# Performance work log

Hardware: AMD Instinct MI355X
Metric: run time of the kernel (lower is better)

## Reference

```python
import jax, jax.numpy as jnp
import numpy as np

D_MODEL = 1024
NUM_HEADS = 16
HEAD_DIM = D_MODEL // NUM_HEADS


def setup_inputs() -> dict:
    key = jax.random.key(0)
    ks = jax.random.split(key, 11)
    B, S = 2, 2048
    sc = 1.0 / np.sqrt(D_MODEL)
    inp = {
        "query": jax.random.normal(ks[0], (B, S, D_MODEL), jnp.float32),
        "key": jax.random.normal(ks[1], (B, S, D_MODEL), jnp.float32),
        "value": jax.random.normal(ks[2], (B, S, D_MODEL), jnp.float32),
        "Wq": jax.random.normal(ks[3], (D_MODEL, D_MODEL), jnp.float32) * sc,
        "bq": jnp.zeros((D_MODEL,), jnp.float32),
        "Wk": jax.random.normal(ks[4], (D_MODEL, D_MODEL), jnp.float32) * sc,
        "bk": jnp.zeros((D_MODEL,), jnp.float32),
        "Wv": jax.random.normal(ks[5], (D_MODEL, D_MODEL), jnp.float32) * sc,
        "bv": jnp.zeros((D_MODEL,), jnp.float32),
        "Wo": jax.random.normal(ks[6], (D_MODEL, D_MODEL), jnp.float32) * sc,
        "bo": jnp.zeros((D_MODEL,), jnp.float32),
    }
    return inp


def _split_heads(x):
    B, S, _ = x.shape
    return x.reshape(B, S, NUM_HEADS, HEAD_DIM).transpose(0, 2, 1, 3)  # [B,H,S,Dh]


def reference(query, key, value, Wq, bq, Wk, bk, Wv, bv, Wo, bo):
    Q = _split_heads(query @ Wq.T + bq)
    K = _split_heads(key @ Wk.T + bk)
    V = _split_heads(value @ Wv.T + bv)
    scores = jnp.einsum("bhqd,bhkd->bhqk", Q, K) / jnp.sqrt(jnp.float32(HEAD_DIM))
    attn = jax.nn.softmax(scores, axis=-1)  # dropout = identity (eval)
    out = jnp.einsum("bhqk,bhkd->bhqd", attn, V)
    B, H, S, Dh = out.shape
    out = out.transpose(0, 2, 1, 3).reshape(B, S, H * Dh)
    return out @ Wo.T + bo
```

## Files before the change

kernel.cpp:

```cpp
#include <hip/hip_runtime.h>
#include <hip/hip_bf16.h>

typedef __attribute__((ext_vector_type(8))) short short8;
typedef __attribute__((ext_vector_type(4))) short short4v;
typedef __attribute__((ext_vector_type(4))) float f32x4;
typedef __attribute__((ext_vector_type(16))) float f32x16;
typedef __attribute__((ext_vector_type(4))) int int4v;
typedef __attribute__((ext_vector_type(2))) int int2v;

#define DEV static __device__ __forceinline__

constexpr int S_LEN   = 2048;
constexpr int DMODEL  = 1024;
constexpr int NHEAD   = 16;
constexpr int DHEAD   = 64;
constexpr int NBATCH  = 2;
constexpr int BHN     = NBATCH * NHEAD;
constexpr int MROWS   = NBATCH * S_LEN;
constexpr int NDIM    = DMODEL;

DEV unsigned short f2b(float f) {
  __hip_bfloat16 h = __float2bfloat16(f);
  return __builtin_bit_cast(unsigned short, h);
}
DEV unsigned pk2(float a, float b) {
  return (unsigned)f2b(a) | ((unsigned)f2b(b) << 16);
}
DEV short8 ld8(const void* p) {
  return *reinterpret_cast<const short8*>(p);
}
DEV f32x4 mfma16(short8 a, short8 b, f32x4 c) {
  return __builtin_amdgcn_mfma_f32_16x16x32_bf16(a, b, c, 0, 0, 0);
}
DEV f32x16 mfma32(short8 a, short8 b, f32x16 c) {
  return __builtin_amdgcn_mfma_f32_32x32x16_bf16(a, b, c, 0, 0, 0);
}
DEV void gload16(const void* g, void* l) {
  __builtin_amdgcn_global_load_lds(
      (const __attribute__((address_space(1))) unsigned*)g,
      (__attribute__((address_space(3))) unsigned*)l, 16, 0, 0);
}

struct CvtArgs {
  const float* src[7];
  unsigned short* dst[7];
  int n4[7];
};

__global__ __launch_bounds__(256) void cvt_bf16(CvtArgs c) {
  const int seg = blockIdx.y;
  const float* __restrict__ s = c.src[seg];
  unsigned short* __restrict__ d = c.dst[seg];
  const int n4 = c.n4[seg];
  for (int i = blockIdx.x * 256 + threadIdx.x; i < n4; i += gridDim.x * 256) {
    f32x4 v = reinterpret_cast<const f32x4*>(s)[i];
    short4v r;
    r[0] = (short)f2b(v[0]); r[1] = (short)f2b(v[1]);
    r[2] = (short)f2b(v[2]); r[3] = (short)f2b(v[3]);
    reinterpret_cast<short4v*>(d)[i] = r;
  }
}

struct GB {
  const unsigned short* A[3];
  const unsigned short* W[3];
  const float* bia[3];
  void* out[3];
  int epi[3];
};

#define WAITV3 asm volatile("s_waitcnt vmcnt(3)" ::: "memory")
#define WAITV0 asm volatile("s_waitcnt vmcnt(0)" ::: "memory")

__global__ __launch_bounds__(256, 4) void gemm_bf16(GB g) {
  const int z = blockIdx.z;
  const unsigned short* __restrict__ A = g.A[z];
  const unsigned short* __restrict__ W = g.W[z];
  const float* __restrict__ bia = g.bia[z];
  const int epi = g.epi[z];
  const int bm = blockIdx.y, bn = blockIdx.x;
  const int tid = threadIdx.x, lane = tid & 63, wid = tid >> 6;
  const int wr = wid >> 1, wc = wid & 1;
  const int fr = lane & 15, gq = lane >> 4;

  __shared__ unsigned short As[3][128][32];
  __shared__ unsigned short Bs[3][64][32];

  f32x4 acc[4][2] = {};

  const int srow = lane >> 2;
  const int scol = ((lane & 3) ^ ((srow >> 1) & 3)) * 16;
  const char* aS = (const char*)A + (size_t)(bm * 128 + wid * 32 + srow) * 2048 + scol;
  const char* bS = (const char*)W + (size_t)(bn * 64 + wid * 16 + srow) * 2048 + scol;

  auto stage = [&](int buf, int kt) {
    const int ko = kt * 64;
    char* a0 = (char*)As[buf] + wid * 2048;
    char* b0 = (char*)Bs[buf] + wid * 1024;
    gload16(aS + ko, a0);
    gload16(aS + (size_t)16 * 2048 + ko, a0 + 1024);
    gload16(bS + ko, b0);
  };

  const int rdo = (gq ^ ((fr >> 1) & 3)) * 8;

  stage(0, 0);
  stage(1, 1);
  for (int kt = 0; kt < 32; ++kt) {
    if (kt < 31) { WAITV3; } else { WAITV0; }
    __builtin_amdgcn_s_barrier();
    if (kt + 2 < 32) stage((kt + 2) % 3, kt + 2);
    const int buf = kt % 3;
    short8 af[4], bf4[2];
#pragma unroll
    for (int i = 0; i < 4; ++i) af[i] = ld8(&As[buf][wr * 64 + i * 16 + fr][rdo]);
#pragma unroll
    for (int j = 0; j < 2; ++j) bf4[j] = ld8(&Bs[buf][wc * 32 + j * 16 + fr][rdo]);
#pragma unroll
    for (int i = 0; i < 4; ++i)
#pragma unroll
      for (int j = 0; j < 2; ++j)
        acc[i][j] = mfma16(af[i], bf4[j], acc[i][j]);
  }

#pragma unroll
  for (int i = 0; i < 4; ++i) {
#pragma unroll
    for (int j = 0; j < 2; ++j) {
#pragma unroll
      for (int r = 0; r < 4; ++r) {
        const int row = bm * 128 + wr * 64 + i * 16 + gq * 4 + r;
        const int col = bn * 64 + wc * 32 + j * 16 + fr;
        float v = acc[i][j][r] + bia[col];
        if (epi == 3) {
          ((float*)g.out[z])[(size_t)row * NDIM + col] = v;
        } else {
          const int b = row >> 11, s = row & (S_LEN - 1);
          const int h = col >> 6,  dh = col & (DHEAD - 1);
          unsigned short* O = (unsigned short*)g.out[z];
          if (epi == 0)      O[((size_t)(b * NHEAD + h) * S_LEN + s) * DHEAD + dh] = f2b(v * 0.125f);
          else if (epi == 1) O[((size_t)(b * NHEAD + h) * S_LEN + s) * DHEAD + dh] = f2b(v);
          else               O[((size_t)(b * NHEAD + h) * DHEAD + dh) * S_LEN + s] = f2b(v);
        }
      }
    }
  }
}

__global__ __launch_bounds__(512, 2) void attn_fwd(
    const unsigned short* __restrict__ Qp,
    const unsigned short* __restrict__ Kp,
    const unsigned short* __restrict__ Vt,
    unsigned short* __restrict__ AO) {
  const int nb = (blockIdx.x & 7) * 64 + (blockIdx.x >> 3);
  const int qt = nb & 15, bh = nb >> 4;
  const int tid = threadIdx.x, lane = tid & 63, wid = tid >> 6;
  const int qw = wid & 3, hw = wid >> 2;
  const int ql = lane & 31, hi = lane >> 5, l7 = lane & 7, l3 = lane >> 3;

  const unsigned short* Qh = Qp + (size_t)bh * S_LEN * DHEAD;
  const char* Kh = (const char*)(Kp + (size_t)bh * S_LEN * DHEAD);
  const char* Vh = (const char*)(Vt + (size_t)bh * DHEAD * S_LEN);

  __shared__ unsigned short Klds[2][2][4096];
  __shared__ unsigned short Vlds[2][2][4096];

  const int q0 = qt * 128 + qw * 32;
  short8 qf[4];
#pragma unroll
  for (int d16 = 0; d16 < 4; ++d16)
    qf[d16] = ld8(Qh + (size_t)(q0 + ql) * DHEAD + d16 * 16 + hi * 8);

  const int swc = (l7 ^ l3) << 4;
  const char* kS = Kh + (size_t)hw * 16 * 8192 + (qw * 16 + l3) * 128 + swc;
  const char* vS = Vh + (size_t)hw * 16 * 128 + (qw * 16 + l3) * 4096 + swc;
  char* kD0 = (char*)Klds[hw][0] + qw * 2048;
  char* vD0 = (char*)Vlds[hw][0] + qw * 2048;
  char* kD1 = (char*)Klds[hw][1] + qw * 2048;
  char* vD1 = (char*)Vlds[hw][1] + qw * 2048;

  int xo[4];
#pragma unroll
  for (int j = 0; j < 4; ++j) xo[j] = ((j * 2 + hi) ^ l7) << 4;

  float m = -1e30f, l = 0.f;
  f32x16 o0 = {}, o1 = {};

  gload16(kS, kD0); gload16(kS + 1024, kD0 + 1024);
  gload16(vS, vD0); gload16(vS + 32768, vD0 + 1024);
  __syncthreads();

  constexpr int NT = S_LEN / 64 / 2;
  for (int kt = 0; kt < NT; ++kt) {
    const int buf = kt & 1;
    if (kt + 1 < NT) {
      const char* kn = kS + (kt + 1) * 8192;
      const char* vn = vS + (kt + 1) * 128;
      char* kD = buf ? kD0 : kD1;
      char* vD = buf ? vD0 : vD1;
      gload16(kn, kD); gload16(kn + 1024, kD + 1024);
      gload16(vn, vD); gload16(vn + 32768, vD + 1024);
    }
    const char* kb = (const char*)Klds[hw][buf] + ql * 128;
    const char* vb = (const char*)Vlds[hw][buf] + ql * 128;

    f32x16 st0 = {}, st1 = {};
#pragma unroll
    for (int d16 = 0; d16 < 4; ++d16) {
      short8 k0 = ld8(kb + xo[d16]);
      short8 k1 = ld8(kb + 4096 + xo[d16]);
      st0 = mfma32(k0, qf[d16], st0);
      st1 = mfma32(k1, qf[d16], st1);
    }

    float t8[8];
#pragma unroll
    for (int r = 0; r < 8; ++r)
      t8[r] = fmaxf(fmaxf(st0[r], st0[r + 8]), fmaxf(st1[r], st1[r + 8]));
#pragma unroll
    for (int s = 4; s; s >>= 1)
#pragma unroll
      for (int r = 0; r < s; ++r) t8[r] = fmaxf(t8[r], t8[r + s]);
    float pm = fmaxf(t8[0], __shfl_xor(t8[0], 32));

    if (!__all(pm <= m + 8.f)) {
      const float mnew = fmaxf(m, pm);
      const float alpha = __expf(m - mnew);
      m = mnew;
      l *= alpha;
#pragma unroll
      for (int r = 0; r < 16; ++r) { o0[r] *= alpha; o1[r] *= alpha; }
    }

#pragma unroll
    for (int r = 0; r < 16; ++r) {
      st0[r] = __expf(st0[r] - m);
      st1[r] = __expf(st1[r] - m);
    }
    float s8[8];
#pragma unroll
    for (int r = 0; r < 8; ++r)
      s8[r] = (st0[r] + st0[r + 8]) + (st1[r] + st1[r + 8]);
#pragma unroll
    for (int s = 4; s; s >>= 1)
#pragma unroll
      for (int r = 0; r < s; ++r) s8[r] += s8[r + s];
    l += s8[0] + __shfl_xor(s8[0], 32);

#pragma unroll
    for (int ks = 0; ks < 4; ++ks) {
      const f32x16& p = (ks < 2) ? st0 : st1;
      const int a = 8 * (ks & 1);
      unsigned w0 = pk2(p[a + 0], p[a + 1]);
      unsigned w1 = pk2(p[a + 2], p[a + 3]);
      unsigned w2 = pk2(p[a + 4], p[a + 5]);
      unsigned w3 = pk2(p[a + 6], p[a + 7]);
      unsigned x0 = (unsigned)__shfl_xor((int)w0, 32);
      unsigned x1 = (unsigned)__shfl_xor((int)w1, 32);
      unsigned x2 = (unsigned)__shfl_xor((int)w2, 32);
      unsigned x3 = (unsigned)__shfl_xor((int)w3, 32);
      int4v pi;
      pi[0] = (int)(hi ? x2 : w0);
      pi[1] = (int)(hi ? x3 : w1);
      pi[2] = (int)(hi ? w2 : x0);
      pi[3] = (int)(hi ? w3 : x1);
      short8 pb = __builtin_bit_cast(short8, pi);
      short8 v0 = ld8(vb + xo[ks]);
      short8 v1 = ld8(vb + 4096 + xo[ks]);
      o0 = mfma32(v0, pb, o0);
      o1 = mfma32(v1, pb, o1);
    }
    __syncthreads();
  }

  float* Kf = (float*)&Klds[0][0][0];
  float* Vf = (float*)&Vlds[0][0][0];
  if (hw == 1) {
#pragma unroll
    for (int r = 0; r < 16; ++r) {
      Kf[qw * 2048 + r * 64 + lane]        = o0[r];
      Kf[qw * 2048 + (16 + r) * 64 + lane] = o1[r];
    }
    Vf[qw * 128 + lane]      = m;
    Vf[qw * 128 + 64 + lane] = l;
  }
  __syncthreads();
  if (hw == 0) {
    const float mb = Vf[qw * 128 + lane];
    const float lb = Vf[qw * 128 + 64 + lane];
    const float M  = fmaxf(m, mb);
    const float wa = __expf(m - M);
    const float wb = __expf(mb - M);
    const float inv = 1.f / (wa * l + wb * lb);
    const int b = bh >> 4, h = bh & 15;
    unsigned short* Op = AO + ((size_t)(b * S_LEN + q0 + ql)) * DMODEL + h * DHEAD;
#pragma unroll
    for (int gidx = 0; gidx < 4; ++gidx) {
      float f0[4], f1[4];
#pragma unroll
      for (int r = 0; r < 4; ++r) {
        const int rr = gidx * 4 + r;
        f0[r] = (wa * o0[rr] + wb * Kf[qw * 2048 + rr * 64 + lane]) * inv;
        f1[r] = (wa * o1[rr] + wb * Kf[qw * 2048 + (16 + rr) * 64 + lane]) * inv;
      }
      int2v s0, s1;
      s0[0] = (int)pk2(f0[0], f0[1]); s0[1] = (int)pk2(f0[2], f0[3]);
      s1[0] = (int)pk2(f1[0], f1[1]); s1[1] = (int)pk2(f1[2], f1[3]);
      *reinterpret_cast<int2v*>(Op + 8 * gidx + 4 * hi)      = s0;
      *reinterpret_cast<int2v*>(Op + 32 + 8 * gidx + 4 * hi) = s1;
    }
  }
}

extern "C" void kernel_launch(void* const* d_in, const int* in_sizes, int n_in,
                              void* d_out, int out_size, void* d_ws, size_t ws_size,
                              hipStream_t stream) {
  const float* query = (const float*)d_in[0];
  const float* key   = (const float*)d_in[1];
  const float* value = (const float*)d_in[2];
  const float* Wq = (const float*)d_in[3];  const float* bq = (const float*)d_in[4];
  const float* Wk = (const float*)d_in[5];  const float* bk = (const float*)d_in[6];
  const float* Wv = (const float*)d_in[7];  const float* bv = (const float*)d_in[8];
  const float* Wo = (const float*)d_in[9];  const float* bo = (const float*)d_in[10];

  const size_t MB = 1024u * 1024u;
  unsigned short* Xb  = (unsigned short*)((char*)d_ws + 0 * MB);
  unsigned short* Wb  = (unsigned short*)((char*)d_ws + 24 * MB);
  unsigned short* Wob = (unsigned short*)((char*)d_ws + 30 * MB);
  unsigned short* Qp  = (unsigned short*)((char*)d_ws + 32 * MB);
  unsigned short* Kp  = (unsigned short*)((char*)d_ws + 40 * MB);
  unsigned short* Vt  = (unsigned short*)((char*)d_ws + 48 * MB);
  unsigned short* AOb = (unsigned short*)((char*)d_ws + 0 * MB);

  const int NACT = MROWS * DMODEL;
  const int NWT  = DMODEL * DMODEL;

  CvtArgs ca;
  ca.src[0] = query; ca.dst[0] = Xb;            ca.n4[0] = NACT / 4;
  ca.src[1] = key;   ca.dst[1] = Xb + NACT;     ca.n4[1] = NACT / 4;
  ca.src[2] = value; ca.dst[2] = Xb + 2 * NACT; ca.n4[2] = NACT / 4;
  ca.src[3] = Wq;    ca.dst[3] = Wb;            ca.n4[3] = NWT / 4;
  ca.src[4] = Wk;    ca.dst[4] = Wb + NWT;      ca.n4[4] = NWT / 4;
  ca.src[5] = Wv;    ca.dst[5] = Wb + 2 * NWT;  ca.n4[5] = NWT / 4;
  ca.src[6] = Wo;    ca.dst[6] = Wob;           ca.n4[6] = NWT / 4;
  cvt_bf16<<<dim3(512, 7), 256, 0, stream>>>(ca);

  GB g1;
  g1.A[0] = Xb;            g1.A[1] = Xb + NACT; g1.A[2] = Xb + 2 * NACT;
  g1.W[0] = Wb;            g1.W[1] = Wb + NWT;  g1.W[2] = Wb + 2 * NWT;
  g1.bia[0] = bq;  g1.bia[1] = bk; g1.bia[2] = bv;
  g1.out[0] = Qp;  g1.out[1] = Kp; g1.out[2] = Vt;
  g1.epi[0] = 0;   g1.epi[1] = 1;  g1.epi[2] = 2;
  gemm_bf16<<<dim3(NDIM / 64, MROWS / 128, 3), 256, 0, stream>>>(g1);

  attn_fwd<<<dim3(BHN * 16), 512, 0, stream>>>(Qp, Kp, Vt, AOb);

  GB g2 = {};
  g2.A[0] = AOb; g2.W[0] = Wob; g2.bia[0] = bo; g2.out[0] = d_out; g2.epi[0] = 3;
  gemm_bf16<<<dim3(NDIM / 64, MROWS / 128, 1), 256, 0, stream>>>(g2);
}
```

Baseline: 161.7 us.

## Hand-schedule LDS reads with priorities and switch softmax to exp2

In both the GEMM and attention kernels, LDS fragment loads now go through inline ds_read_b128 with precomputed addresses. Each batch of loads ends in an explicit lgkmcnt wait, and the MFMA blocks are wrapped in s_setprio. The attention loop drops its end-of-iteration __syncthreads and instead does a vmcnt wait plus barrier at the top of each iteration, with all K and V fragments loaded into registers before their MFMAs. The softmax moves to exp2 by folding log2(e) into the Q scaling, and the rescale threshold is adjusted to match. The aim is to cut barrier count, address arithmetic and exp cost and to overlap work across waves, at the cost of extra register pressure and fragile hand-placed waitcnts.

```diff
diff --git a/kernel.cpp b/kernel.cpp
--- a/kernel.cpp
+++ b/kernel.cpp
@@ -19,6 +19,8 @@
 constexpr int MROWS   = NBATCH * S_LEN;
 constexpr int NDIM    = DMODEL;
 
+constexpr float QSCALE = 0.125f * 1.442695041f;
+
 DEV unsigned short f2b(float f) {
   __hip_bfloat16 h = __float2bfloat16(f);
   return __builtin_bit_cast(unsigned short, h);
@@ -40,6 +42,15 @@
       (const __attribute__((address_space(1))) unsigned*)g,
       (__attribute__((address_space(3))) unsigned*)l, 16, 0, 0);
 }
+DEV short8 dsread16(unsigned addr) {
+  short8 d;
+  asm volatile("ds_read_b128 %0, %1" : "=v"(d) : "v"(addr));
+  return d;
+}
+#define WAITV(n)  asm volatile("s_waitcnt vmcnt(" #n ")" ::: "memory")
+#define WAITLGK(n) do { asm volatile("s_waitcnt lgkmcnt(" #n ")" ::: "memory"); \
+                        __builtin_amdgcn_sched_barrier(0); } while (0)
+DEV unsigned ldsaddr(const void* p) { return (unsigned)(uintptr_t)p; }
 
 struct CvtArgs {
   const float* src[7];
@@ -69,9 +80,6 @@
   int epi[3];
 };
 
-#define WAITV3 asm volatile("s_waitcnt vmcnt(3)" ::: "memory")
-#define WAITV0 asm volatile("s_waitcnt vmcnt(0)" ::: "memory")
-
 __global__ __launch_bounds__(256, 4) void gemm_bf16(GB g) {
   const int z = blockIdx.z;
   const unsigned short* __restrict__ A = g.A[z];
@@ -103,24 +111,33 @@
   };
 
   const int rdo = (gq ^ ((fr >> 1) & 3)) * 8;
+  unsigned aAd[4], bAd[2];
+#pragma unroll
+  for (int i = 0; i < 4; ++i) aAd[i] = ldsaddr(&As[0][wr * 64 + i * 16 + fr][rdo]);
+#pragma unroll
+  for (int j = 0; j < 2; ++j) bAd[j] = ldsaddr(&Bs[0][wc * 32 + j * 16 + fr][rdo]);
 
   stage(0, 0);
   stage(1, 1);
   for (int kt = 0; kt < 32; ++kt) {
-    if (kt < 31) { WAITV3; } else { WAITV0; }
+    if (kt < 31) { WAITV(3); } else { WAITV(0); }
     __builtin_amdgcn_s_barrier();
     if (kt + 2 < 32) stage((kt + 2) % 3, kt + 2);
-    const int buf = kt % 3;
+    const unsigned ao = (unsigned)(kt % 3) * 8192;
+    const unsigned bo = (unsigned)(kt % 3) * 4096;
     short8 af[4], bf4[2];
 #pragma unroll
-    for (int i = 0; i < 4; ++i) af[i] = ld8(&As[buf][wr * 64 + i * 16 + fr][rdo]);
-#pragma unroll
-    for (int j = 0; j < 2; ++j) bf4[j] = ld8(&Bs[buf][wc * 32 + j * 16 + fr][rdo]);
+    for (int i = 0; i < 4; ++i) af[i] = dsread16(aAd[i] + ao);
+#pragma unroll
+    for (int j = 0; j < 2; ++j) bf4[j] = dsread16(bAd[j] + bo);
+    WAITLGK(0);
+    __builtin_amdgcn_s_setprio(1);
 #pragma unroll
     for (int i = 0; i < 4; ++i)
 #pragma unroll
       for (int j = 0; j < 2; ++j)
         acc[i][j] = mfma16(af[i], bf4[j], acc[i][j]);
+    __builtin_amdgcn_s_setprio(0);
   }
 
 #pragma unroll
@@ -138,7 +155,7 @@
           const int b = row >> 11, s = row & (S_LEN - 1);
           const int h = col >> 6,  dh = col & (DHEAD - 1);
           unsigned short* O = (unsigned short*)g.out[z];
-          if (epi == 0)      O[((size_t)(b * NHEAD + h) * S_LEN + s) * DHEAD + dh] = f2b(v * 0.125f);
+          if (epi == 0)      O[((size_t)(b * NHEAD + h) * S_LEN + s) * DHEAD + dh] = f2b(v * QSCALE);
           else if (epi == 1) O[((size_t)(b * NHEAD + h) * S_LEN + s) * DHEAD + dh] = f2b(v);
           else               O[((size_t)(b * NHEAD + h) * DHEAD + dh) * S_LEN + s] = f2b(v);
         }
@@ -183,15 +200,19 @@
 #pragma unroll
   for (int j = 0; j < 4; ++j) xo[j] = ((j * 2 + hi) ^ l7) << 4;
 
+  const unsigned kB = ldsaddr(&Klds[hw][0][0]) + ql * 128;
+  const unsigned vB = ldsaddr(&Vlds[hw][0][0]) + ql * 128;
+
   float m = -1e30f, l = 0.f;
   f32x16 o0 = {}, o1 = {};
 
   gload16(kS, kD0); gload16(kS + 1024, kD0 + 1024);
   gload16(vS, vD0); gload16(vS + 32768, vD0 + 1024);
-  __syncthreads();
 
   constexpr int NT = S_LEN / 64 / 2;
   for (int kt = 0; kt < NT; ++kt) {
+    WAITV(0);
+    __builtin_amdgcn_s_barrier();
     const int buf = kt & 1;
     if (kt + 1 < NT) {
       const char* kn = kS + (kt + 1) * 8192;
@@ -201,17 +222,23 @@
       gload16(kn, kD); gload16(kn + 1024, kD + 1024);
       gload16(vn, vD); gload16(vn + 32768, vD + 1024);
     }
-    const char* kb = (const char*)Klds[hw][buf] + ql * 128;
-    const char* vb = (const char*)Vlds[hw][buf] + ql * 128;
-
+    const unsigned ko = (unsigned)buf * 8192;
+
+    short8 kf[8];
+#pragma unroll
+    for (int d = 0; d < 4; ++d) {
+      kf[d]     = dsread16(kB + ko + xo[d]);
+      kf[4 + d] = dsread16(kB + ko + 4096 + xo[d]);
+    }
+    WAITLGK(0);
     f32x16 st0 = {}, st1 = {};
-#pragma unroll
-    for (int d16 = 0; d16 < 4; ++d16) {
-      short8 k0 = ld8(kb + xo[d16]);
-      short8 k1 = ld8(kb + 4096 + xo[d16]);
-      st0 = mfma32(k0, qf[d16], st0);
-      st1 = mfma32(k1, qf[d16], st1);
-    }
+    __builtin_amdgcn_s_setprio(1);
+#pragma unroll
+    for (int d = 0; d < 4; ++d) {
+      st0 = mfma32(kf[d], qf[d], st0);
+      st1 = mfma32(kf[4 + d], qf[d], st1);
+    }
+    __builtin_amdgcn_s_setprio(0);
 
     float t8[8];
 #pragma unroll
@@ -223,9 +250,9 @@
       for (int r = 0; r < s; ++r) t8[r] = fmaxf(t8[r], t8[r + s]);
     float pm = fmaxf(t8[0], __shfl_xor(t8[0], 32));
 
-    if (!__all(pm <= m + 8.f)) {
+    if (!__all(pm <= m + 11.54f)) {
       const float mnew = fmaxf(m, pm);
-      const float alpha = __expf(m - mnew);
+      const float alpha = exp2f(m - mnew);
       m = mnew;
       l *= alpha;
 #pragma unroll
@@ -234,8 +261,8 @@
 
 #pragma unroll
     for (int r = 0; r < 16; ++r) {
-      st0[r] = __expf(st0[r] - m);
-      st1[r] = __expf(st1[r] - m);
+      st0[r] = exp2f(st0[r] - m);
+      st1[r] = exp2f(st1[r] - m);
     }
     float s8[8];
 #pragma unroll
@@ -247,6 +274,14 @@
       for (int r = 0; r < s; ++r) s8[r] += s8[r + s];
     l += s8[0] + __shfl_xor(s8[0], 32);
 
+    short8 vf[8];
+#pragma unroll
+    for (int ks = 0; ks < 4; ++ks) {
+      vf[ks]     = dsread16(vB + ko + xo[ks]);
+      vf[4 + ks] = dsread16(vB + ko + 4096 + xo[ks]);
+    }
+    WAITLGK(0);
+    __builtin_amdgcn_s_setprio(1);
 #pragma unroll
     for (int ks = 0; ks < 4; ++ks) {
       const f32x16& p = (ks < 2) ? st0 : st1;
@@ -265,13 +300,13 @@
       pi[2] = (int)(hi ? w2 : x0);
       pi[3] = (int)(hi ? w3 : x1);
       short8 pb = __builtin_bit_cast(short8, pi);
-      short8 v0 = ld8(vb + xo[ks]);
-      short8 v1 = ld8(vb + 4096 + xo[ks]);
-      o0 = mfma32(v0, pb, o0);
-      o1 = mfma32(v1, pb, o1);
-    }
-    __syncthreads();
-  }
+      o0 = mfma32(vf[ks], pb, o0);
+      o1 = mfma32(vf[4 + ks], pb, o1);
+    }
+    __builtin_amdgcn_s_setprio(0);
+  }
+
+  __syncthreads();
 
   float* Kf = (float*)&Klds[0][0][0];
   float* Vf = (float*)&Vlds[0][0][0];
@@ -289,8 +324,8 @@
     const float mb = Vf[qw * 128 + lane];
     const float lb = Vf[qw * 128 + 64 + lane];
     const float M  = fmaxf(m, mb);
-    const float wa = __expf(m - M);
-    const float wb = __expf(mb - M);
+    const float wa = exp2f(m - M);
+    const float wb = exp2f(mb - M);
     const float inv = 1.f / (wa * l + wb * lb);
     const int b = bh >> 4, h = bh & 15;
     unsigned short* Op = AO + ((size_t)(b * S_LEN + q0 + ql)) * DMODEL + h * DHEAD;
```

New measurement: 172.4 us. +6.6%, slower.
